# Kernel tuning notes

Measured on AMD Instinct MI355X. Metric: run time of the kernel, lower is better.

## Reference

```python
import jax, jax.numpy as jnp
import numpy as np

B, L, H, NH, P = 4, 1024, 1024, 16, 2048
HD = H // NH


def setup_inputs() -> dict:
    key = jax.random.key(0)
    ks = jax.random.split(key, 6)
    x = jax.random.normal(ks[0], (B, L, H), dtype=jnp.float32)
    # torch.nn.Linear weights are [out, in]
    Wqkv = jax.random.normal(ks[1], (3 * H, H), dtype=jnp.float32) * 0.02
    bqkv = jnp.zeros((3 * H,), dtype=jnp.float32)
    Wo = jax.random.normal(ks[2], (H, H), dtype=jnp.float32) * 0.02
    bo = jnp.zeros((H,), dtype=jnp.float32)
    Er = jax.random.normal(ks[3], (NH, P, HD), dtype=jnp.float32)
    # causal mask: True where attention is disallowed (masked_fill semantics)
    mask = jnp.triu(jnp.ones((L, L), dtype=bool), k=1)
    return {"x": x, "mask": mask, "Wqkv": Wqkv, "bqkv": bqkv,
            "Wo": Wo, "bo": bo, "Er": Er}


def reference(x, mask, Wqkv, bqkv, Wo, bo, Er):
    b, l, d = x.shape
    nh, p, hd = Er.shape
    qkv = x @ Wqkv.T + bqkv                      # [b, l, 3d]
    q, k, v = jnp.split(qkv, 3, axis=-1)
    q = q.reshape(b, l, nh, hd).transpose(0, 2, 1, 3)   # [b, nh, l, hd]
    k = k.reshape(b, l, nh, hd).transpose(0, 2, 1, 3)
    v = v.reshape(b, l, nh, hd).transpose(0, 2, 1, 3)

    scores = jnp.einsum('bnlh,bnkh->bnlk', q, k) / jnp.sqrt(
        jnp.asarray(hd, dtype=x.dtype))

    # relative positions (j - i), torch negative-index wraparound -> mod p
    pos = jnp.arange(l)
    rel = (pos[None, :] - pos[:, None]) % p      # [l, l] in [0, p)
    # Equivalent to einsum('bnlh,rnlkh->bnlk', q, Er[:, rel][None]) but
    # computed as q @ Er^T over all positions then gathered (same math,
    # avoids materializing the [nh, l, l, hd] tensor).
    QEr_full = jnp.einsum('bnlh,nph->bnlp', q, Er)       # [b, nh, l, p]
    i_idx = pos[:, None]                          # broadcasts with rel
    QEr = QEr_full[:, :, i_idx, rel]              # [b, nh, l, l]

    a = scores + QEr
    a = jnp.where(mask, -jnp.inf, a)
    a = jax.nn.softmax(a, axis=-1)                # dropout: eval mode (identity)

    out = jnp.einsum('bnlk,bnkh->bnlh', a, v)     # [b, nh, l, hd]
    out = out.transpose(0, 2, 1, 3).reshape(b, l, d)
    return out @ Wo.T + bo
```

## Files before the change

kernel.cpp:

```cpp
#include <hip/hip_runtime.h>

typedef unsigned short u16;
typedef __bf16 bf16x8 __attribute__((ext_vector_type(8)));
typedef unsigned short u16x8 __attribute__((ext_vector_type(8)));
typedef float f32x4 __attribute__((ext_vector_type(4)));

#define MFMA16(a, b, c) __builtin_amdgcn_mfma_f32_16x16x32_bf16((a), (b), (c), 0, 0, 0)

__device__ __forceinline__ u16 f2b(float f) {
  unsigned u = __float_as_uint(f);
  u += 0x7fffu + ((u >> 16) & 1u);
  return (u16)(u >> 16);
}
__device__ __forceinline__ float b2f(u16 h) {
  return __uint_as_float(((unsigned)h) << 16);
}

__global__ void cvt_bf16(const float* __restrict__ src, u16* __restrict__ dst, int n4) {
  int i = blockIdx.x * blockDim.x + threadIdx.x;
  if (i >= n4) return;
  float4 v = *(const float4*)(src + (size_t)i * 4);
  *(ushort4*)(dst + (size_t)i * 4) = make_ushort4(f2b(v.x), f2b(v.y), f2b(v.z), f2b(v.w));
}

__global__ void build_F(const float* __restrict__ Er, u16* __restrict__ Fb) {
  int i = blockIdx.x * blockDim.x + threadIdx.x;
  int base = i * 4;
  int d = base & 63;
  int m = (base >> 6) & 1023;
  int n = base >> 16;
  int sm = (2048 - m) & 2047;
  float4 v = *(const float4*)(Er + ((size_t)(n * 2048 + sm) * 64 + d));
  *(ushort4*)(Fb + (size_t)base) = make_ushort4(f2b(v.x), f2b(v.y), f2b(v.z), f2b(v.w));
}

__global__ __launch_bounds__(256) void gemm_qkv(const u16* __restrict__ A, const u16* __restrict__ Bw,
                                                const float* __restrict__ bias,
                                                u16* __restrict__ Qo, u16* __restrict__ Ko,
                                                u16* __restrict__ Vo) {
  __shared__ u16 As[4][128][8];
  __shared__ u16 Bs[4][128][8];
  const int m0 = blockIdx.y * 128, n0 = blockIdx.x * 128;
  const int t = threadIdx.x, lane = t & 63, w = t >> 6;
  const int wr = w >> 1, wc = w & 1;
  const int l16 = lane & 15, lg = lane >> 4;
  f32x4 acc[4][4] = {};
  const int ch0 = t * 2, ch1 = t * 2 + 1;
  const int r0 = ch0 >> 2, g0 = ch0 & 3, r1 = ch1 >> 2, g1 = ch1 & 3;

  u16x8 pa0 = *(const u16x8*)&A[(size_t)(m0 + r0) * 1024 + g0 * 8];
  u16x8 pa1 = *(const u16x8*)&A[(size_t)(m0 + r1) * 1024 + g1 * 8];
  u16x8 pb0 = *(const u16x8*)&Bw[(size_t)(n0 + r0) * 1024 + g0 * 8];
  u16x8 pb1 = *(const u16x8*)&Bw[(size_t)(n0 + r1) * 1024 + g1 * 8];

  for (int k0 = 0; k0 < 1024; k0 += 32) {
    *(u16x8*)&As[g0][r0][0] = pa0;
    *(u16x8*)&As[g1][r1][0] = pa1;
    *(u16x8*)&Bs[g0][r0][0] = pb0;
    *(u16x8*)&Bs[g1][r1][0] = pb1;
    __syncthreads();
    if (k0 + 32 < 1024) {
      int k1 = k0 + 32;
      pa0 = *(const u16x8*)&A[(size_t)(m0 + r0) * 1024 + k1 + g0 * 8];
      pa1 = *(const u16x8*)&A[(size_t)(m0 + r1) * 1024 + k1 + g1 * 8];
      pb0 = *(const u16x8*)&Bw[(size_t)(n0 + r0) * 1024 + k1 + g0 * 8];
      pb1 = *(const u16x8*)&Bw[(size_t)(n0 + r1) * 1024 + k1 + g1 * 8];
    }
    bf16x8 af[4], bfr[4];
#pragma unroll
    for (int m = 0; m < 4; ++m) af[m] = *(const bf16x8*)&As[lg][wr * 64 + m * 16 + l16][0];
#pragma unroll
    for (int n = 0; n < 4; ++n) bfr[n] = *(const bf16x8*)&Bs[lg][wc * 64 + n * 16 + l16][0];
#pragma unroll
    for (int m = 0; m < 4; ++m)
#pragma unroll
      for (int n = 0; n < 4; ++n) acc[m][n] = MFMA16(af[m], bfr[n], acc[m][n]);
    __syncthreads();
  }

#pragma unroll
  for (int n = 0; n < 4; ++n) {
    int col = n0 + wc * 64 + n * 16 + l16;
    float bq = bias[col];
    int which = col >> 10;
    int h = col & 1023;
    int head = h >> 6, d = h & 63;
    u16* dst = which == 0 ? Qo : (which == 1 ? Ko : Vo);
    float scale = which == 1 ? 0.125f : 1.0f;
#pragma unroll
    for (int m = 0; m < 4; ++m) {
#pragma unroll
      for (int r = 0; r < 4; ++r) {
        int row = m0 + wr * 64 + m * 16 + lg * 4 + r;
        int b = row >> 10, ii = row & 1023;
        float v = (acc[m][n][r] + bq) * scale;
        dst[(size_t)(((b * 16 + head) << 10) + ii) * 64 + d] = f2b(v);
      }
    }
  }
}

__global__ __launch_bounds__(256) void gemm_out(const u16* __restrict__ A, const u16* __restrict__ Bw,
                                                const float* __restrict__ bias, float* __restrict__ Co) {
  __shared__ u16 As[4][128][8];
  __shared__ u16 Bs[4][128][8];
  const int m0 = blockIdx.y * 128, n0 = blockIdx.x * 128;
  const int t = threadIdx.x, lane = t & 63, w = t >> 6;
  const int wr = w >> 1, wc = w & 1;
  const int l16 = lane & 15, lg = lane >> 4;
  f32x4 acc[4][4] = {};
  const int ch0 = t * 2, ch1 = t * 2 + 1;
  const int r0 = ch0 >> 2, g0 = ch0 & 3, r1 = ch1 >> 2, g1 = ch1 & 3;

  u16x8 pa0 = *(const u16x8*)&A[(size_t)(m0 + r0) * 1024 + g0 * 8];
  u16x8 pa1 = *(const u16x8*)&A[(size_t)(m0 + r1) * 1024 + g1 * 8];
  u16x8 pb0 = *(const u16x8*)&Bw[(size_t)(n0 + r0) * 1024 + g0 * 8];
  u16x8 pb1 = *(const u16x8*)&Bw[(size_t)(n0 + r1) * 1024 + g1 * 8];

  for (int k0 = 0; k0 < 1024; k0 += 32) {
    *(u16x8*)&As[g0][r0][0] = pa0;
    *(u16x8*)&As[g1][r1][0] = pa1;
    *(u16x8*)&Bs[g0][r0][0] = pb0;
    *(u16x8*)&Bs[g1][r1][0] = pb1;
    __syncthreads();
    if (k0 + 32 < 1024) {
      int k1 = k0 + 32;
      pa0 = *(const u16x8*)&A[(size_t)(m0 + r0) * 1024 + k1 + g0 * 8];
      pa1 = *(const u16x8*)&A[(size_t)(m0 + r1) * 1024 + k1 + g1 * 8];
      pb0 = *(const u16x8*)&Bw[(size_t)(n0 + r0) * 1024 + k1 + g0 * 8];
      pb1 = *(const u16x8*)&Bw[(size_t)(n0 + r1) * 1024 + k1 + g1 * 8];
    }
    bf16x8 af[4], bfr[4];
#pragma unroll
    for (int m = 0; m < 4; ++m) af[m] = *(const bf16x8*)&As[lg][wr * 64 + m * 16 + l16][0];
#pragma unroll
    for (int n = 0; n < 4; ++n) bfr[n] = *(const bf16x8*)&Bs[lg][wc * 64 + n * 16 + l16][0];
#pragma unroll
    for (int m = 0; m < 4; ++m)
#pragma unroll
      for (int n = 0; n < 4; ++n) acc[m][n] = MFMA16(af[m], bfr[n], acc[m][n]);
    __syncthreads();
  }

#pragma unroll
  for (int n = 0; n < 4; ++n) {
    int col = n0 + wc * 64 + n * 16 + l16;
    float bq = bias[col];
#pragma unroll
    for (int m = 0; m < 4; ++m) {
#pragma unroll
      for (int r = 0; r < 4; ++r) {
        int row = m0 + wr * 64 + m * 16 + lg * 4 + r;
        Co[(size_t)row * 1024 + col] = acc[m][n][r] + bq;
      }
    }
  }
}

__global__ __launch_bounds__(256) void attn_kernel(const u16* __restrict__ Qg, const u16* __restrict__ Kg,
                                                   const u16* __restrict__ Vg, const u16* __restrict__ Fg,
                                                   u16* __restrict__ AO) {
  __shared__ u16 Kl[8][64][8];
  __shared__ u16 Vt[8][64][8];
  __shared__ u16 Fl[8][128][8];
  __shared__ u16 Bnd[4][16][132];
  __shared__ u16 Pl[4][8][16][8];

  const int bn = blockIdx.x;
  const int b = bn >> 4, n = bn & 15;
  const int qt = 15 - (int)blockIdx.y;
  const int i0 = qt * 64;
  const int t = threadIdx.x, lane = t & 63, w = t >> 6;
  const int l16 = lane & 15, lg = lane >> 4;

  bf16x8 qf[2];
  {
    const u16* qp = &Qg[(size_t)((bn << 10) + i0 + (w << 4) + l16) * 64 + lg * 8];
    qf[0] = *(const bf16x8*)qp;
    qf[1] = *(const bf16x8*)(qp + 32);
  }

  float mrun[4], lrun[4];
  f32x4 ao[4] = {};
#pragma unroll
  for (int r = 0; r < 4; ++r) { mrun[r] = -3.0e38f; lrun[r] = 0.0f; }

  for (int jt = 0; jt <= qt; ++jt) {
    const int j0 = jt * 64;
    const int mbase = i0 - j0 - 63;
    const bool diag = (jt == qt);

#pragma unroll
    for (int s = 0; s < 2; ++s) {
      int ch = t * 2 + s;
      int j = ch >> 3, kg = ch & 7;
      *(u16x8*)&Kl[kg][j][0] = *(const u16x8*)&Kg[(size_t)((bn << 10) + j0 + j) * 64 + kg * 8];
      u16x8 vv = *(const u16x8*)&Vg[(size_t)((bn << 10) + j0 + j) * 64 + kg * 8];
#pragma unroll
      for (int e = 0; e < 8; ++e) Vt[j >> 3][kg * 8 + e][j & 7] = vv[e];
    }
#pragma unroll
    for (int s = 0; s < 4; ++s) {
      int ch = t * 4 + s;
      int tr = ch >> 3, kg = ch & 7;
      int mrow = mbase + tr;
      mrow = mrow < 0 ? 0 : (mrow > 1023 ? 1023 : mrow);
      *(u16x8*)&Fl[kg][tr][0] = *(const u16x8*)&Fg[(size_t)((n << 10) + mrow) * 64 + kg * 8];
    }
    __syncthreads();

    f32x4 sc[4] = {};
#pragma unroll
    for (int kk = 0; kk < 2; ++kk)
#pragma unroll
      for (int nn = 0; nn < 4; ++nn) {
        bf16x8 kb = *(const bf16x8*)&Kl[lg + kk * 4][nn * 16 + l16][0];
        sc[nn] = MFMA16(qf[kk], kb, sc[nn]);
      }
    f32x4 bb[8] = {};
#pragma unroll
    for (int kk = 0; kk < 2; ++kk)
#pragma unroll
      for (int nt = 0; nt < 8; ++nt) {
        bf16x8 fb = *(const bf16x8*)&Fl[lg + kk * 4][nt * 16 + l16][0];
        bb[nt] = MFMA16(qf[kk], fb, bb[nt]);
      }
#pragma unroll
    for (int nt = 0; nt < 8; ++nt)
#pragma unroll
      for (int r = 0; r < 4; ++r) Bnd[w][lg * 4 + r][nt * 16 + l16] = f2b(bb[nt][r]);
    __syncthreads();

    float pv[4][4];
#pragma unroll
    for (int r = 0; r < 4; ++r) {
      int rowstrip = (w << 4) + lg * 4 + r;
      float stmp[4];
      float mx = -3.0e38f;
#pragma unroll
      for (int nn = 0; nn < 4; ++nn) {
        int tt = rowstrip - (nn * 16 + l16) + 63;
        float s = sc[nn][r] + b2f(Bnd[w][lg * 4 + r][tt]);
        if (diag && tt < 63) s = -1.0e30f;
        stmp[nn] = s;
        mx = fmaxf(mx, s);
      }
#pragma unroll
      for (int off = 1; off < 16; off <<= 1) mx = fmaxf(mx, __shfl_xor(mx, off));
      float mnew = fmaxf(mrun[r], mx);
      float scl = __expf(mrun[r] - mnew);
      float rs = 0.0f;
#pragma unroll
      for (int nn = 0; nn < 4; ++nn) {
        pv[nn][r] = __expf(stmp[nn] - mnew);
        rs += pv[nn][r];
      }
#pragma unroll
      for (int off = 1; off < 16; off <<= 1) rs += __shfl_xor(rs, off);
      lrun[r] = lrun[r] * scl + rs;
      mrun[r] = mnew;
#pragma unroll
      for (int nd = 0; nd < 4; ++nd) ao[nd][r] *= scl;
    }

#pragma unroll
    for (int nn = 0; nn < 4; ++nn)
#pragma unroll
      for (int r = 0; r < 4; ++r) {
        int jl = nn * 16 + l16;
        Pl[w][jl >> 3][lg * 4 + r][jl & 7] = f2b(pv[nn][r]);
      }
    __syncthreads();
#pragma unroll
    for (int kk = 0; kk < 2; ++kk) {
      bf16x8 pa = *(const bf16x8*)&Pl[w][lg + kk * 4][l16][0];
#pragma unroll
      for (int nd = 0; nd < 4; ++nd) {
        bf16x8 vb = *(const bf16x8*)&Vt[lg + kk * 4][nd * 16 + l16][0];
        ao[nd] = MFMA16(pa, vb, ao[nd]);
      }
    }
    __syncthreads();
  }

#pragma unroll
  for (int nd = 0; nd < 4; ++nd)
#pragma unroll
    for (int r = 0; r < 4; ++r) {
      int i = i0 + (w << 4) + lg * 4 + r;
      int d = nd * 16 + l16;
      float v = ao[nd][r] / lrun[r];
      AO[(size_t)((b << 10) + i) * 1024 + n * 64 + d] = f2b(v);
    }
}

extern "C" void kernel_launch(void* const* d_in, const int* in_sizes, int n_in,
                              void* d_out, int out_size, void* d_ws, size_t ws_size,
                              hipStream_t stream) {
  (void)in_sizes; (void)n_in; (void)out_size; (void)ws_size;
  const float* x    = (const float*)d_in[0];
  const float* Wqkv = (const float*)d_in[2];
  const float* bqkv = (const float*)d_in[3];
  const float* Wo   = (const float*)d_in[4];
  const float* bo   = (const float*)d_in[5];
  const float* Er   = (const float*)d_in[6];
  float* out = (float*)d_out;

  char* p = (char*)d_ws;
  u16* xb    = (u16*)p; p += (size_t)4096 * 1024 * 2;
  u16* wqkvb = (u16*)p; p += (size_t)3072 * 1024 * 2;
  u16* wob   = (u16*)p; p += (size_t)1024 * 1024 * 2;
  u16* Fb    = (u16*)p; p += (size_t)16 * 1024 * 64 * 2;
  u16* Qb    = (u16*)p; p += (size_t)64 * 1024 * 64 * 2;
  u16* Kb    = (u16*)p; p += (size_t)64 * 1024 * 64 * 2;
  u16* Vb    = (u16*)p; p += (size_t)64 * 1024 * 64 * 2;
  u16* AO    = (u16*)p; p += (size_t)4096 * 1024 * 2;

  cvt_bf16<<<4096, 256, 0, stream>>>(x, xb, 1048576);
  cvt_bf16<<<3072, 256, 0, stream>>>(Wqkv, wqkvb, 786432);
  cvt_bf16<<<1024, 256, 0, stream>>>(Wo, wob, 262144);
  build_F<<<1024, 256, 0, stream>>>(Er, Fb);
  gemm_qkv<<<dim3(24, 32), 256, 0, stream>>>(xb, wqkvb, bqkv, Qb, Kb, Vb);
  attn_kernel<<<dim3(64, 16), 256, 0, stream>>>(Qb, Kb, Vb, Fb, AO);
  gemm_out<<<dim3(8, 32), 256, 0, stream>>>(AO, wob, bo, out);
}
```

Before: 159.5 us.

## Pre-transpose V, swizzle attention LDS tiles, trim relative-bias band, use wave-local fences

Adds a separate kernel that writes V transposed to global memory, so the attention kernel no longer scatters V element by element into LDS. K, V, F and P tiles now use XOR-swizzled row-major LDS layouts to avoid bank conflicts. Each wave computes only the 5 relative-position column tiles it needs instead of 8, and reads the band with packed 32-bit loads. Two block-wide barriers become wave-local waitcnt fences, since Bnd and Pl are per-wave. The cost is an extra launch and a global round trip for V.

```diff
diff --git a/kernel.cpp b/kernel.cpp
--- a/kernel.cpp
+++ b/kernel.cpp
@@ -6,6 +6,11 @@
 typedef float f32x4 __attribute__((ext_vector_type(4)));
 
 #define MFMA16(a, b, c) __builtin_amdgcn_mfma_f32_16x16x32_bf16((a), (b), (c), 0, 0, 0)
+
+#define WAVE_LDS_FENCE() do { \
+  asm volatile("s_waitcnt lgkmcnt(0)" ::: "memory"); \
+  __builtin_amdgcn_sched_barrier(0); \
+} while (0)
 
 __device__ __forceinline__ u16 f2b(float f) {
   unsigned u = __float_as_uint(f);
@@ -32,6 +37,31 @@
   int sm = (2048 - m) & 2047;
   float4 v = *(const float4*)(Er + ((size_t)(n * 2048 + sm) * 64 + d));
   *(ushort4*)(Fb + (size_t)base) = make_ushort4(f2b(v.x), f2b(v.y), f2b(v.z), f2b(v.w));
+}
+
+__global__ __launch_bounds__(256) void transpose_v(const u16* __restrict__ V, u16* __restrict__ Vt) {
+  __shared__ u16 T[4096];
+  const int bn = blockIdx.x, i0 = blockIdx.y * 64;
+  const int t = threadIdx.x;
+#pragma unroll
+  for (int s = 0; s < 2; ++s) {
+    int ch = t + 256 * s;
+    int i = ch >> 3, c = ch & 7;
+    u16x8 v = *(const u16x8*)&V[(size_t)((bn << 10) + i0 + i) * 64 + c * 8];
+#pragma unroll
+    for (int e = 0; e < 8; ++e) {
+      int d = c * 8 + e;
+      T[d * 64 + ((((i >> 3) ^ (d & 7) ^ ((d >> 3) & 7)) & 7) << 3) + (i & 7)] = v[e];
+    }
+  }
+  __syncthreads();
+#pragma unroll
+  for (int s = 0; s < 2; ++s) {
+    int ch = t + 256 * s;
+    int d = ch >> 3, cc = ch & 7;
+    u16x8 o = *(const u16x8*)&T[d * 64 + (((cc ^ (d & 7) ^ ((d >> 3) & 7)) & 7) << 3)];
+    *(u16x8*)&Vt[(size_t)((bn << 6) + d) * 1024 + i0 + cc * 8] = o;
+  }
 }
 
 __global__ __launch_bounds__(256) void gemm_qkv(const u16* __restrict__ A, const u16* __restrict__ Bw,
@@ -158,13 +188,13 @@
 }
 
 __global__ __launch_bounds__(256) void attn_kernel(const u16* __restrict__ Qg, const u16* __restrict__ Kg,
-                                                   const u16* __restrict__ Vg, const u16* __restrict__ Fg,
+                                                   const u16* __restrict__ Vtg, const u16* __restrict__ Fg,
                                                    u16* __restrict__ AO) {
-  __shared__ u16 Kl[8][64][8];
-  __shared__ u16 Vt[8][64][8];
-  __shared__ u16 Fl[8][128][8];
-  __shared__ u16 Bnd[4][16][132];
-  __shared__ u16 Pl[4][8][16][8];
+  __shared__ u16 Kl[4096];
+  __shared__ u16 Vl[4096];
+  __shared__ u16 Fl[8192];
+  __shared__ u16 Bnd[4][16][84];
+  __shared__ u16 Pl[4][1024];
 
   const int bn = blockIdx.x;
   const int b = bn >> 4, n = bn & 15;
@@ -192,20 +222,21 @@
 
 #pragma unroll
     for (int s = 0; s < 2; ++s) {
-      int ch = t * 2 + s;
-      int j = ch >> 3, kg = ch & 7;
-      *(u16x8*)&Kl[kg][j][0] = *(const u16x8*)&Kg[(size_t)((bn << 10) + j0 + j) * 64 + kg * 8];
-      u16x8 vv = *(const u16x8*)&Vg[(size_t)((bn << 10) + j0 + j) * 64 + kg * 8];
-#pragma unroll
-      for (int e = 0; e < 8; ++e) Vt[j >> 3][kg * 8 + e][j & 7] = vv[e];
+      int ch = t + 256 * s;
+      int r = ch >> 3, c = ch & 7;
+      u16x8 kv = *(const u16x8*)&Kg[(size_t)((bn << 10) + j0 + r) * 64 + c * 8];
+      *(u16x8*)&Kl[r * 64 + (((c ^ (r & 7)) & 7) << 3)] = kv;
+      u16x8 vv = *(const u16x8*)&Vtg[(size_t)((bn << 6) + r) * 1024 + j0 + c * 8];
+      *(u16x8*)&Vl[r * 64 + (((c ^ (r & 7)) & 7) << 3)] = vv;
     }
 #pragma unroll
     for (int s = 0; s < 4; ++s) {
-      int ch = t * 4 + s;
-      int tr = ch >> 3, kg = ch & 7;
-      int mrow = mbase + tr;
+      int ch = t + 256 * s;
+      int r = ch >> 3, c = ch & 7;
+      int mrow = mbase + r;
       mrow = mrow < 0 ? 0 : (mrow > 1023 ? 1023 : mrow);
-      *(u16x8*)&Fl[kg][tr][0] = *(const u16x8*)&Fg[(size_t)((n << 10) + mrow) * 64 + kg * 8];
+      u16x8 fv = *(const u16x8*)&Fg[(size_t)((n << 10) + mrow) * 64 + c * 8];
+      *(u16x8*)&Fl[r * 64 + (((c ^ (r & 7)) & 7) << 3)] = fv;
     }
     __syncthreads();
 
@@ -214,34 +245,41 @@
     for (int kk = 0; kk < 2; ++kk)
 #pragma unroll
       for (int nn = 0; nn < 4; ++nn) {
-        bf16x8 kb = *(const bf16x8*)&Kl[lg + kk * 4][nn * 16 + l16][0];
+        int jr = nn * 16 + l16;
+        bf16x8 kb = *(const bf16x8*)&Kl[jr * 64 + ((((lg + 4 * kk) ^ (jr & 7)) & 7) << 3)];
         sc[nn] = MFMA16(qf[kk], kb, sc[nn]);
       }
-    f32x4 bb[8] = {};
+    f32x4 bb[5] = {};
 #pragma unroll
     for (int kk = 0; kk < 2; ++kk)
 #pragma unroll
-      for (int nt = 0; nt < 8; ++nt) {
-        bf16x8 fb = *(const bf16x8*)&Fl[lg + kk * 4][nt * 16 + l16][0];
-        bb[nt] = MFMA16(qf[kk], fb, bb[nt]);
-      }
-#pragma unroll
-    for (int nt = 0; nt < 8; ++nt)
-#pragma unroll
-      for (int r = 0; r < 4; ++r) Bnd[w][lg * 4 + r][nt * 16 + l16] = f2b(bb[nt][r]);
-    __syncthreads();
-
+      for (int ct = 0; ct < 5; ++ct) {
+        int trow = (w << 4) + ct * 16 + l16;
+        bf16x8 fb = *(const bf16x8*)&Fl[trow * 64 + ((((lg + 4 * kk) ^ (trow & 7)) & 7) << 3)];
+        bb[ct] = MFMA16(qf[kk], fb, bb[ct]);
+      }
+#pragma unroll
+    for (int ct = 0; ct < 5; ++ct)
+#pragma unroll
+      for (int r = 0; r < 4; ++r)
+        Bnd[w][lg * 4 + r][ct * 16 + l16] = f2b(bb[ct][r]);
+    WAVE_LDS_FENCE();
+
+    const unsigned* bw = (const unsigned*)&Bnd[w][0][0];
     float pv[4][4];
 #pragma unroll
     for (int r = 0; r < 4; ++r) {
-      int rowstrip = (w << 4) + lg * 4 + r;
+      int il = lg * 4 + r;
+      int c0 = il - l16 + 63;
+      int u0 = il * 84 + c0;
+      int sh = (u0 & 1) << 4;
       float stmp[4];
       float mx = -3.0e38f;
 #pragma unroll
       for (int nn = 0; nn < 4; ++nn) {
-        int tt = rowstrip - (nn * 16 + l16) + 63;
-        float s = sc[nn][r] + b2f(Bnd[w][lg * 4 + r][tt]);
-        if (diag && tt < 63) s = -1.0e30f;
+        unsigned dv = bw[(u0 >> 1) - 8 * nn];
+        float s = sc[nn][r] + b2f((u16)((dv >> sh) & 0xffffu));
+        if (diag && (c0 - 16 * nn + (w << 4) < 63)) s = -1.0e30f;
         stmp[nn] = s;
         mx = fmaxf(mx, s);
       }
@@ -267,16 +305,17 @@
     for (int nn = 0; nn < 4; ++nn)
 #pragma unroll
       for (int r = 0; r < 4; ++r) {
-        int jl = nn * 16 + l16;
-        Pl[w][jl >> 3][lg * 4 + r][jl & 7] = f2b(pv[nn][r]);
-      }
-    __syncthreads();
+        int i = lg * 4 + r, j = nn * 16 + l16;
+        Pl[w][i * 64 + ((((j >> 3) ^ (i & 7)) & 7) << 3) + (j & 7)] = f2b(pv[nn][r]);
+      }
+    WAVE_LDS_FENCE();
 #pragma unroll
     for (int kk = 0; kk < 2; ++kk) {
-      bf16x8 pa = *(const bf16x8*)&Pl[w][lg + kk * 4][l16][0];
+      bf16x8 pa = *(const bf16x8*)&Pl[w][l16 * 64 + ((((lg + 4 * kk) ^ (l16 & 7)) & 7) << 3)];
 #pragma unroll
       for (int nd = 0; nd < 4; ++nd) {
-        bf16x8 vb = *(const bf16x8*)&Vt[lg + kk * 4][nd * 16 + l16][0];
+        int dr = nd * 16 + l16;
+        bf16x8 vb = *(const bf16x8*)&Vl[dr * 64 + ((((lg + 4 * kk) ^ (dr & 7)) & 7) << 3)];
         ao[nd] = MFMA16(pa, vb, ao[nd]);
       }
     }
@@ -314,6 +353,7 @@
   u16* Qb    = (u16*)p; p += (size_t)64 * 1024 * 64 * 2;
   u16* Kb    = (u16*)p; p += (size_t)64 * 1024 * 64 * 2;
   u16* Vb    = (u16*)p; p += (size_t)64 * 1024 * 64 * 2;
+  u16* Vtb   = (u16*)p; p += (size_t)64 * 1024 * 64 * 2;
   u16* AO    = (u16*)p; p += (size_t)4096 * 1024 * 2;
 
   cvt_bf16<<<4096, 256, 0, stream>>>(x, xb, 1048576);
@@ -321,6 +361,7 @@
   cvt_bf16<<<1024, 256, 0, stream>>>(Wo, wob, 262144);
   build_F<<<1024, 256, 0, stream>>>(Er, Fb);
   gemm_qkv<<<dim3(24, 32), 256, 0, stream>>>(xb, wqkvb, bqkv, Qb, Kb, Vb);
-  attn_kernel<<<dim3(64, 16), 256, 0, stream>>>(Qb, Kb, Vb, Fb, AO);
+  transpose_v<<<dim3(64, 16), 256, 0, stream>>>(Vb, Vtb);
+  attn_kernel<<<dim3(64, 16), 256, 0, stream>>>(Qb, Kb, Vtb, Fb, AO);
   gemm_out<<<dim3(8, 32), 256, 0, stream>>>(AO, wob, bo, out);
 }
```

Result: faster. 154.3 us (-3.3%).
